# Kernel optimization log

Measured on AMD Instinct MI355X. Metric: run time of the kernel, lower is better.

## Reference

```python
import jax, jax.numpy as jnp
import numpy as np
from jax import lax

DIM = 128
HEADS = 8
B, H, W = 8, 128, 128


def conv1x1(w, x):
    # w: [out_c, in_c], x: [b, in_c, h, w]
    return jnp.einsum('oc,bchw->bohw', w, x)


def setup_inputs() -> dict:
    key = jax.random.key(0)
    ks = jax.random.split(key, 12)
    s = 0.02
    return {
        'x': jax.random.normal(ks[0], (B, DIM, H, W), dtype=jnp.float32),
        'W_qkv': jax.random.normal(ks[1], (3 * DIM, DIM), dtype=jnp.float32) * s,
        'W_dw': jax.random.normal(ks[2], (DIM, 1, 3, 3), dtype=jnp.float32) * s,
        'W_proj_s': jax.random.normal(ks[3], (DIM, DIM), dtype=jnp.float32) * s,
        'scale_s': jnp.ones((HEADS, 1, 1), dtype=jnp.float32),
        'W_ff1': jax.random.normal(ks[4], (DIM, DIM), dtype=jnp.float32) * s,
        'W_ff2': jax.random.normal(ks[5], (DIM, DIM), dtype=jnp.float32) * s,
        'W_proj_f': jax.random.normal(ks[6], (DIM, DIM), dtype=jnp.float32) * s,
        'W_gsf': jax.random.normal(ks[7], (DIM, DIM), dtype=jnp.float32) * s,
        'b_gsf': jnp.zeros((DIM,), dtype=jnp.float32),
        'W_gfs': jax.random.normal(ks[8], (DIM, DIM), dtype=jnp.float32) * s,
        'b_gfs': jnp.zeros((DIM,), dtype=jnp.float32),
    }


def reference(x, W_qkv, W_dw, W_proj_s, scale_s, W_ff1, W_ff2, W_proj_f,
              W_gsf, b_gsf, W_gfs, b_gfs):
    b, c, h, w = x.shape
    head = HEADS
    ch = c // head

    # --- channel self-attention branch ---
    qkv = conv1x1(W_qkv, x)                      # [b, 3c, h, w]
    q_s, k_s, v_s = jnp.split(qkv, 3, axis=1)
    v_s_conv = lax.conv_general_dilated(
        v_s, W_dw, window_strides=(1, 1), padding='SAME',
        feature_group_count=c,
        dimension_numbers=('NCHW', 'OIHW', 'NCHW'))  # depthwise 3x3

    q = q_s.reshape(b, head, ch, h * w)
    k = k_s.reshape(b, head, ch, h * w)
    v = v_s.reshape(b, head, ch, h * w)
    attn = jax.nn.softmax(jnp.einsum('bhcn,bhdn->bhcd', q, k) * scale_s, axis=-1)
    out_s = jnp.einsum('bhcd,bhdn->bhcn', attn, v).reshape(b, c, h, w)
    out_s = conv1x1(W_proj_s, out_s + v_s_conv)

    # --- frequency filter branch ---
    xf = jnp.fft.rfft2(x, norm='ortho')          # complex [b,c,h,w//2+1]
    spatial_weights = conv1x1(W_ff2, jax.nn.gelu(conv1x1(W_ff1, x), approximate=False))
    freq_weights = jnp.fft.rfft2(spatial_weights, norm='ortho')
    out_f = jnp.fft.irfft2(xf * freq_weights, s=(h, w), norm='ortho')
    out_f = conv1x1(W_proj_f, out_f)

    # --- sigmoid-gated fusion ---
    gate_f = jax.nn.sigmoid(conv1x1(W_gsf, out_s) + b_gsf[:, None, None])
    gate_s = jax.nn.sigmoid(conv1x1(W_gfs, out_f) + b_gfs[:, None, None])
    return x + out_s * gate_s + out_f * gate_f
```

## Files before the change

### kernel.cpp

```cpp
#include <hip/hip_runtime.h>
#include <hip/hip_bf16.h>
#include <math.h>

#define HW 16384

typedef __attribute__((ext_vector_type(8))) short bf16x8;
typedef __attribute__((ext_vector_type(4))) float f32x4;

__device__ __forceinline__ unsigned short f2bf(float a)
{
    __hip_bfloat16 h = __float2bfloat16(a);
    return __builtin_bit_cast(unsigned short, h);
}
__device__ __forceinline__ unsigned f2bf_pk(float a, float b)
{
    return (unsigned)f2bf(a) | ((unsigned)f2bf(b) << 16);
}
__device__ __forceinline__ float bf2f(unsigned short u)
{
    return __uint_as_float(((unsigned)u) << 16);
}
__device__ __forceinline__ float sigmoidf_(float v) { return 1.f / (1.f + expf(-v)); }

__device__ __forceinline__ float2 cmul(float2 a, float2 b)
{
    return make_float2(a.x * b.x - a.y * b.y, a.x * b.y + a.y * b.x);
}

__global__ __launch_bounds__(256)
void wprep_k(const float* __restrict__ w0, const float* __restrict__ w1,
             const float* __restrict__ w2, const float* __restrict__ w3,
             const float* __restrict__ w4, const float* __restrict__ w5,
             const float* __restrict__ w6, int4* __restrict__ Wbf4)
{
    int m = blockIdx.x >> 3;
    int slot = (blockIdx.x & 7) * 256 + threadIdx.x;
    const float* src;
    switch (m) {
        case 0: src = w0; break;
        case 1: src = w1; break;
        case 2: src = w2; break;
        case 3: src = w3; break;
        case 4: src = w4; break;
        case 5: src = w5; break;
        default: src = w6; break;
    }
    int o = slot >> 4;
    int c16 = (slot & 15) ^ (o & 7);
    const float* p = src + o * 128 + c16 * 8;
    int4 pk;
    pk.x = f2bf_pk(p[0], p[1]); pk.y = f2bf_pk(p[2], p[3]);
    pk.z = f2bf_pk(p[4], p[5]); pk.w = f2bf_pk(p[6], p[7]);
    Wbf4[m * 2048 + slot] = pk;
}

__global__ __launch_bounds__(256)
void head_k(const float* __restrict__ x, const int4* __restrict__ wv,
            const int4* __restrict__ w1, const int4* __restrict__ w2,
            unsigned short* __restrict__ V, unsigned short* __restrict__ swb)
{
    __shared__ short WL[128 * 128];
    __shared__ short XLx[64 * 128];
    __shared__ short XM[64 * 128];
    int t = threadIdx.x;
    int gb = blockIdx.x;
    int b = gb >> 8;
    int n0 = (gb & 255) << 6;

    #pragma unroll
    for (int it = 0; it < 8; ++it)
        ((int4*)WL)[it * 256 + t] = wv[it * 256 + t];

    const float* inb = x + (size_t)b * 128 * HW + n0;
    int nl = t & 63;
    #pragma unroll
    for (int it = 0; it < 4; ++it) {
        int c8 = (t >> 6) + it * 4;
        float v[8];
        #pragma unroll
        for (int j = 0; j < 8; ++j) v[j] = inb[(size_t)(c8 * 8 + j) * HW + nl];
        int4 p;
        p.x = f2bf_pk(v[0], v[1]); p.y = f2bf_pk(v[2], v[3]);
        p.z = f2bf_pk(v[4], v[5]); p.w = f2bf_pk(v[6], v[7]);
        ((int4*)XLx)[nl * 16 + (c8 ^ (nl & 7))] = p;
    }
    __syncthreads();

    int l = t & 63, w = t >> 6, kg = l >> 4, l15 = l & 15, l7 = l15 & 7;

    f32x4 acc[2][4];
    #pragma unroll
    for (int mf = 0; mf < 2; ++mf)
        #pragma unroll
        for (int nf = 0; nf < 4; ++nf) acc[mf][nf] = (f32x4){0.f, 0.f, 0.f, 0.f};
    #pragma unroll
    for (int ks = 0; ks < 4; ++ks) {
        int ch = ks * 4 + kg;
        bf16x8 A0 = ((const bf16x8*)WL)[(w * 32 + l15) * 16 + (ch ^ l7)];
        bf16x8 A1 = ((const bf16x8*)WL)[(w * 32 + 16 + l15) * 16 + (ch ^ l7)];
        #pragma unroll
        for (int nf = 0; nf < 4; ++nf) {
            bf16x8 Bf = ((const bf16x8*)XLx)[(nf * 16 + l15) * 16 + (ch ^ l7)];
            acc[0][nf] = __builtin_amdgcn_mfma_f32_16x16x32_bf16(A0, Bf, acc[0][nf], 0, 0, 0);
            acc[1][nf] = __builtin_amdgcn_mfma_f32_16x16x32_bf16(A1, Bf, acc[1][nf], 0, 0, 0);
        }
    }
    #pragma unroll
    for (int mf = 0; mf < 2; ++mf)
        #pragma unroll
        for (int nf = 0; nf < 4; ++nf)
            #pragma unroll
            for (int i = 0; i < 4; ++i) {
                int row = w * 32 + mf * 16 + kg * 4 + i;
                int col = n0 + nf * 16 + l15;
                V[((size_t)b * 128 + row) * HW + col] = f2bf(acc[mf][nf][i]);
            }
    __syncthreads();

    #pragma unroll
    for (int it = 0; it < 8; ++it)
        ((int4*)WL)[it * 256 + t] = w1[it * 256 + t];
    __syncthreads();

    #pragma unroll
    for (int mf = 0; mf < 2; ++mf)
        #pragma unroll
        for (int nf = 0; nf < 4; ++nf) acc[mf][nf] = (f32x4){0.f, 0.f, 0.f, 0.f};
    #pragma unroll
    for (int ks = 0; ks < 4; ++ks) {
        int ch = ks * 4 + kg;
        bf16x8 A0 = ((const bf16x8*)WL)[(w * 32 + l15) * 16 + (ch ^ l7)];
        bf16x8 A1 = ((const bf16x8*)WL)[(w * 32 + 16 + l15) * 16 + (ch ^ l7)];
        #pragma unroll
        for (int nf = 0; nf < 4; ++nf) {
            bf16x8 Bf = ((const bf16x8*)XLx)[(nf * 16 + l15) * 16 + (ch ^ l7)];
            acc[0][nf] = __builtin_amdgcn_mfma_f32_16x16x32_bf16(A0, Bf, acc[0][nf], 0, 0, 0);
            acc[1][nf] = __builtin_amdgcn_mfma_f32_16x16x32_bf16(A1, Bf, acc[1][nf], 0, 0, 0);
        }
    }
    __syncthreads();

    #pragma unroll
    for (int it = 0; it < 8; ++it)
        ((int4*)WL)[it * 256 + t] = w2[it * 256 + t];
    #pragma unroll
    for (int mf = 0; mf < 2; ++mf)
        #pragma unroll
        for (int nf = 0; nf < 4; ++nf) {
            float g4[4];
            #pragma unroll
            for (int i = 0; i < 4; ++i) {
                float v = acc[mf][nf][i];
                g4[i] = 0.5f * v * (1.0f + erff(v * 0.70710678118654752f));
            }
            int col = nf * 16 + l15;
            int r0 = w * 32 + mf * 16 + kg * 4;
            int octet = r0 >> 3;
            uint2 pk2;
            pk2.x = f2bf_pk(g4[0], g4[1]);
            pk2.y = f2bf_pk(g4[2], g4[3]);
            ((uint2*)XM)[(col * 16 + (octet ^ (col & 7))) * 2 + (kg & 1)] = pk2;
        }
    __syncthreads();

    f32x4 acc2[2][4];
    #pragma unroll
    for (int mf = 0; mf < 2; ++mf)
        #pragma unroll
        for (int nf = 0; nf < 4; ++nf) acc2[mf][nf] = (f32x4){0.f, 0.f, 0.f, 0.f};
    #pragma unroll
    for (int ks = 0; ks < 4; ++ks) {
        int ch = ks * 4 + kg;
        bf16x8 A0 = ((const bf16x8*)WL)[(w * 32 + l15) * 16 + (ch ^ l7)];
        bf16x8 A1 = ((const bf16x8*)WL)[(w * 32 + 16 + l15) * 16 + (ch ^ l7)];
        #pragma unroll
        for (int nf = 0; nf < 4; ++nf) {
            bf16x8 Bf = ((const bf16x8*)XM)[(nf * 16 + l15) * 16 + (ch ^ l7)];
            acc2[0][nf] = __builtin_amdgcn_mfma_f32_16x16x32_bf16(A0, Bf, acc2[0][nf], 0, 0, 0);
            acc2[1][nf] = __builtin_amdgcn_mfma_f32_16x16x32_bf16(A1, Bf, acc2[1][nf], 0, 0, 0);
        }
    }
    #pragma unroll
    for (int mf = 0; mf < 2; ++mf)
        #pragma unroll
        for (int nf = 0; nf < 4; ++nf)
            #pragma unroll
            for (int i = 0; i < 4; ++i) {
                int row = w * 32 + mf * 16 + kg * 4 + i;
                int col = n0 + nf * 16 + l15;
                swb[((size_t)b * 128 + row) * HW + col] = f2bf(acc2[mf][nf][i]);
            }
}

__global__ __launch_bounds__(256)
void conv_mfma_bf_k(const unsigned short* __restrict__ in,
                    const int4* __restrict__ wbf,
                    unsigned short* __restrict__ out)
{
    __shared__ short WL[128 * 128];
    __shared__ short XL[64 * 128];
    int t = threadIdx.x;
    int gb = blockIdx.x;
    int b = gb >> 8;
    int n0 = (gb & 255) << 6;

    #pragma unroll
    for (int it = 0; it < 8; ++it)
        ((int4*)WL)[it * 256 + t] = wbf[it * 256 + t];

    const unsigned short* inb = in + (size_t)b * 128 * HW + n0;
    int nl = t & 63;
    #pragma unroll
    for (int it = 0; it < 4; ++it) {
        int c8 = (t >> 6) + it * 4;
        unsigned u[8];
        #pragma unroll
        for (int j = 0; j < 8; ++j) u[j] = inb[(size_t)(c8 * 8 + j) * HW + nl];
        int4 p;
        p.x = (int)(u[0] | (u[1] << 16)); p.y = (int)(u[2] | (u[3] << 16));
        p.z = (int)(u[4] | (u[5] << 16)); p.w = (int)(u[6] | (u[7] << 16));
        ((int4*)XL)[nl * 16 + (c8 ^ (nl & 7))] = p;
    }
    __syncthreads();

    int l = t & 63, w = t >> 6, kg = l >> 4, l15 = l & 15, l7 = l15 & 7;
    f32x4 acc[2][4];
    #pragma unroll
    for (int mf = 0; mf < 2; ++mf)
        #pragma unroll
        for (int nf = 0; nf < 4; ++nf) acc[mf][nf] = (f32x4){0.f, 0.f, 0.f, 0.f};
    #pragma unroll
    for (int ks = 0; ks < 4; ++ks) {
        int ch = ks * 4 + kg;
        bf16x8 A0 = ((const bf16x8*)WL)[(w * 32 + l15) * 16 + (ch ^ l7)];
        bf16x8 A1 = ((const bf16x8*)WL)[(w * 32 + 16 + l15) * 16 + (ch ^ l7)];
        #pragma unroll
        for (int nf = 0; nf < 4; ++nf) {
            bf16x8 Bf = ((const bf16x8*)XL)[(nf * 16 + l15) * 16 + (ch ^ l7)];
            acc[0][nf] = __builtin_amdgcn_mfma_f32_16x16x32_bf16(A0, Bf, acc[0][nf], 0, 0, 0);
            acc[1][nf] = __builtin_amdgcn_mfma_f32_16x16x32_bf16(A1, Bf, acc[1][nf], 0, 0, 0);
        }
    }
    #pragma unroll
    for (int mf = 0; mf < 2; ++mf)
        #pragma unroll
        for (int nf = 0; nf < 4; ++nf)
            #pragma unroll
            for (int i = 0; i < 4; ++i) {
                int row = w * 32 + mf * 16 + kg * 4 + i;
                int col = n0 + nf * 16 + l15;
                out[((size_t)b * 128 + row) * HW + col] = f2bf(acc[mf][nf][i]);
            }
}

__global__ __launch_bounds__(256)
void dwconv_k(const unsigned short* __restrict__ V, const float* __restrict__ Wdw,
              unsigned short* __restrict__ vcb)
{
    int tid = blockIdx.x * 256 + threadIdx.x;
    int e4 = tid & 4095;
    int bc = tid >> 12;
    int c = bc & 127;
    int y = e4 >> 5;
    int x0 = (e4 & 31) << 2;
    const unsigned short* vin = V + (size_t)bc * HW;
    float wf[9];
    #pragma unroll
    for (int i = 0; i < 9; ++i) wf[i] = Wdw[c * 9 + i];
    float a0 = 0.f, a1 = 0.f, a2 = 0.f, a3 = 0.f;
    #pragma unroll
    for (int dy = 0; dy < 3; ++dy) {
        int yy = y + dy - 1;
        if (yy < 0 || yy > 127) continue;
        const unsigned short* r = vin + yy * 128;
        uint2 mu = *(const uint2*)(r + x0);
        float m0 = bf2f((unsigned short)(mu.x & 0xFFFF));
        float m1 = bf2f((unsigned short)(mu.x >> 16));
        float m2 = bf2f((unsigned short)(mu.y & 0xFFFF));
        float m3 = bf2f((unsigned short)(mu.y >> 16));
        float left  = (x0 > 0)   ? bf2f(r[x0 - 1]) : 0.f;
        float right = (x0 < 124) ? bf2f(r[x0 + 4]) : 0.f;
        float w0 = wf[dy * 3], w1 = wf[dy * 3 + 1], w2 = wf[dy * 3 + 2];
        a0 += w0 * left + w1 * m0 + w2 * m1;
        a1 += w0 * m0   + w1 * m1 + w2 * m2;
        a2 += w0 * m1   + w1 * m2 + w2 * m3;
        a3 += w0 * m2   + w1 * m3 + w2 * right;
    }
    uint2 r2;
    r2.x = f2bf_pk(a0, a1);
    r2.y = f2bf_pk(a2, a3);
    *(uint2*)(vcb + (size_t)bc * HW + y * 128 + x0) = r2;
}

__global__ __launch_bounds__(256)
void gram_mfma_k(const float* __restrict__ x, float* __restrict__ Gp)
{
    __shared__ short XL[128 * 128];
    int t = threadIdx.x;
    int blk = blockIdx.x;
    int b = blk >> 5, ks = blk & 31;
    const float* xb = x + (size_t)b * 128 * HW + ks * 512;
    int l = t & 63, w = t >> 6, kg = l >> 4, l15 = l & 15, l7 = l15 & 7;

    f32x4 acc[2][8];
    #pragma unroll
    for (int mf = 0; mf < 2; ++mf)
        #pragma unroll
        for (int nf = 0; nf < 8; ++nf) acc[mf][nf] = (f32x4){0.f, 0.f, 0.f, 0.f};

    for (int kc = 0; kc < 4; ++kc) {
        __syncthreads();
        #pragma unroll
        for (int it = 0; it < 8; ++it) {
            int g = it * 256 + t;
            int row = g >> 4, oct = g & 15;
            const float* p = xb + (size_t)row * HW + kc * 128 + oct * 8;
            int4 pk;
            pk.x = f2bf_pk(p[0], p[1]); pk.y = f2bf_pk(p[2], p[3]);
            pk.z = f2bf_pk(p[4], p[5]); pk.w = f2bf_pk(p[6], p[7]);
            ((int4*)XL)[row * 16 + (oct ^ (row & 7))] = pk;
        }
        __syncthreads();
        #pragma unroll
        for (int s = 0; s < 4; ++s) {
            int oct = s * 4 + kg;
            bf16x8 A0 = ((const bf16x8*)XL)[(w * 32 + l15) * 16 + (oct ^ l7)];
            bf16x8 A1 = ((const bf16x8*)XL)[(w * 32 + 16 + l15) * 16 + (oct ^ l7)];
            #pragma unroll
            for (int nf = 0; nf < 8; ++nf) {
                bf16x8 Bf = ((const bf16x8*)XL)[(nf * 16 + l15) * 16 + (oct ^ l7)];
                acc[0][nf] = __builtin_amdgcn_mfma_f32_16x16x32_bf16(A0, Bf, acc[0][nf], 0, 0, 0);
                acc[1][nf] = __builtin_amdgcn_mfma_f32_16x16x32_bf16(A1, Bf, acc[1][nf], 0, 0, 0);
            }
        }
    }
    float* gp = Gp + (size_t)blk * 16384;
    #pragma unroll
    for (int mf = 0; mf < 2; ++mf)
        #pragma unroll
        for (int nf = 0; nf < 8; ++nf)
            #pragma unroll
            for (int i = 0; i < 4; ++i) {
                int row = w * 32 + mf * 16 + kg * 4 + i;
                int col = nf * 16 + l15;
                gp[row * 128 + col] = acc[mf][nf][i];
            }
}

__global__ void gram_reduce_k(const float* __restrict__ Gp, float* __restrict__ G)
{
    int idx = blockIdx.x * 256 + threadIdx.x;
    int b = idx >> 14;
    int ij = idx & 16383;
    const float* gp = Gp + (size_t)(b * 32) * 16384 + ij;
    float s = 0.f;
    #pragma unroll
    for (int ks = 0; ks < 32; ++ks) s += gp[(size_t)ks * 16384];
    G[idx] = s;
}

__global__ __launch_bounds__(256)
void attn_s2_k(const float* __restrict__ G, const float* __restrict__ Wqkv,
               const float* __restrict__ scale, float* __restrict__ S)
{
    __shared__ float Wq[16][129];
    __shared__ float Wk[16][129];
    __shared__ float Ts[16][129];
    int bh = blockIdx.x;
    int b = bh >> 3, h = bh & 7;
    int t = threadIdx.x;
    #pragma unroll
    for (int i = 0; i < 8; ++i) {
        int idx = t + i * 256;
        int r = idx >> 7, ci = idx & 127;
        Wq[r][ci] = Wqkv[(size_t)(h * 16 + r) * 128 + ci];
        Wk[r][ci] = Wqkv[(size_t)(128 + h * 16 + r) * 128 + ci];
    }
    __syncthreads();
    const float* Gb = G + (size_t)b * 16384;
    #pragma unroll
    for (int i = 0; i < 8; ++i) {
        int idx = t + i * 256;
        int c = idx >> 7, col = idx & 127;
        float s = 0.f;
        #pragma unroll 8
        for (int ci = 0; ci < 128; ++ci)
            s += Wq[c][ci] * Gb[ci * 128 + col];
        Ts[c][col] = s;
    }
    __syncthreads();
    int c = t >> 4, d = t & 15;
    float s = 0.f;
    #pragma unroll 8
    for (int col = 0; col < 128; ++col)
        s += Ts[c][col] * Wk[d][col];
    s *= scale[h];
    float m = s;
    #pragma unroll
    for (int w = 1; w < 16; w <<= 1)
        m = fmaxf(m, __shfl_xor(m, w, 64));
    float e = expf(s - m);
    float sum = e;
    #pragma unroll
    for (int w = 1; w < 16; w <<= 1)
        sum += __shfl_xor(sum, w, 64);
    S[(size_t)bh * 256 + t] = e / sum;
}

__global__ __launch_bounds__(256)
void proj_s_pv_k(const unsigned short* __restrict__ V,
                 const unsigned short* __restrict__ vcb,
                 const float* __restrict__ S, const int4* __restrict__ wbf,
                 unsigned short* __restrict__ out_s)
{
    __shared__ short WL[128 * 128];
    __shared__ short XL[64 * 128];
    __shared__ float SL[2048];
    int t = threadIdx.x;
    int gb = blockIdx.x;
    int b = gb >> 8;
    int n0 = (gb & 255) << 6;

    #pragma unroll
    for (int it = 0; it < 8; ++it)
        ((int4*)WL)[it * 256 + t] = wbf[it * 256 + t];
    #pragma unroll
    for (int i = 0; i < 8; ++i)
        SL[i * 256 + t] = S[(size_t)b * 2048 + i * 256 + t];
    __syncthreads();

    int col = t & 63, w = t >> 6;
    #pragma unroll
    for (int hh = 0; hh < 2; ++hh) {
        int h = w * 2 + hh;
        float v[16];
        #pragma unroll
        for (int d = 0; d < 16; ++d)
            v[d] = bf2f(V[((size_t)(b * 128 + h * 16 + d)) * HW + n0 + col]);
        float o[16];
        #pragma unroll
        for (int c = 0; c < 16; ++c) {
            const float* sl = SL + h * 256 + c * 16;
            float s = 0.f;
            #pragma unroll
            for (int d = 0; d < 16; ++d) s += sl[d] * v[d];
            o[c] = s + bf2f(vcb[((size_t)(b * 128 + h * 16 + c)) * HW + n0 + col]);
        }
        #pragma unroll
        for (int oc = 0; oc < 2; ++oc) {
            int octet = h * 2 + oc;
            int4 p;
            p.x = f2bf_pk(o[oc * 8 + 0], o[oc * 8 + 1]);
            p.y = f2bf_pk(o[oc * 8 + 2], o[oc * 8 + 3]);
            p.z = f2bf_pk(o[oc * 8 + 4], o[oc * 8 + 5]);
            p.w = f2bf_pk(o[oc * 8 + 6], o[oc * 8 + 7]);
            ((int4*)XL)[col * 16 + (octet ^ (col & 7))] = p;
        }
    }
    __syncthreads();

    int l = t & 63, kg = l >> 4, l15 = l & 15, l7 = l15 & 7;
    f32x4 acc[2][4];
    #pragma unroll
    for (int mf = 0; mf < 2; ++mf)
        #pragma unroll
        for (int nf = 0; nf < 4; ++nf) acc[mf][nf] = (f32x4){0.f, 0.f, 0.f, 0.f};
    #pragma unroll
    for (int ks = 0; ks < 4; ++ks) {
        int ch = ks * 4 + kg;
        bf16x8 A0 = ((const bf16x8*)WL)[(w * 32 + l15) * 16 + (ch ^ l7)];
        bf16x8 A1 = ((const bf16x8*)WL)[(w * 32 + 16 + l15) * 16 + (ch ^ l7)];
        #pragma unroll
        for (int nf = 0; nf < 4; ++nf) {
            bf16x8 Bf = ((const bf16x8*)XL)[(nf * 16 + l15) * 16 + (ch ^ l7)];
            acc[0][nf] = __builtin_amdgcn_mfma_f32_16x16x32_bf16(A0, Bf, acc[0][nf], 0, 0, 0);
            acc[1][nf] = __builtin_amdgcn_mfma_f32_16x16x32_bf16(A1, Bf, acc[1][nf], 0, 0, 0);
        }
    }
    #pragma unroll
    for (int mf = 0; mf < 2; ++mf)
        #pragma unroll
        for (int nf = 0; nf < 4; ++nf)
            #pragma unroll
            for (int i = 0; i < 4; ++i) {
                int row = w * 32 + mf * 16 + kg * 4 + i;
                int colg = n0 + nf * 16 + l15;
                out_s[((size_t)b * 128 + row) * HW + colg] = f2bf(acc[mf][nf][i]);
            }
}

__global__ __launch_bounds__(256)
void fuse2_k(const float* __restrict__ x, const unsigned short* __restrict__ outs,
             const unsigned short* __restrict__ outf,
             const int4* __restrict__ wgsf_bf, const float* __restrict__ bgsf,
             const int4* __restrict__ wgfs_bf, const float* __restrict__ bgfs,
             float* __restrict__ out)
{
    __shared__ short WS[64 * 128];
    __shared__ short WF[64 * 128];
    __shared__ short XS[64 * 128];
    __shared__ short XF[64 * 128];
    int t = threadIdx.x;
    int gb = blockIdx.x;
    int xcd = gb & 7, ii = gb >> 3;
    int T = xcd * 256 + (ii >> 1);
    int half = ii & 1;
    int b = T >> 8;
    int n0 = (T & 255) << 6;

    #pragma unroll
    for (int it = 0; it < 4; ++it) {
        ((int4*)WS)[it * 256 + t] = wgsf_bf[half * 1024 + it * 256 + t];
        ((int4*)WF)[it * 256 + t] = wgfs_bf[half * 1024 + it * 256 + t];
    }
    const unsigned short* sb = outs + (size_t)b * 128 * HW + n0;
    const unsigned short* fb = outf + (size_t)b * 128 * HW + n0;
    int nl = t & 63;
    #pragma unroll
    for (int it = 0; it < 4; ++it) {
        int c8 = (t >> 6) + it * 4;
        unsigned us[8], uf[8];
        #pragma unroll
        for (int j = 0; j < 8; ++j) {
            size_t a = (size_t)(c8 * 8 + j) * HW + nl;
            us[j] = sb[a];
            uf[j] = fb[a];
        }
        int4 ps, pf;
        ps.x = (int)(us[0] | (us[1] << 16)); ps.y = (int)(us[2] | (us[3] << 16));
        ps.z = (int)(us[4] | (us[5] << 16)); ps.w = (int)(us[6] | (us[7] << 16));
        pf.x = (int)(uf[0] | (uf[1] << 16)); pf.y = (int)(uf[2] | (uf[3] << 16));
        pf.z = (int)(uf[4] | (uf[5] << 16)); pf.w = (int)(uf[6] | (uf[7] << 16));
        ((int4*)XS)[nl * 16 + (c8 ^ (nl & 7))] = ps;
        ((int4*)XF)[nl * 16 + (c8 ^ (nl & 7))] = pf;
    }
    __syncthreads();

    int l = t & 63, w = t >> 6, kg = l >> 4, l15 = l & 15, l7 = l15 & 7;
    f32x4 aS[4], aF[4];
    #pragma unroll
    for (int nf = 0; nf < 4; ++nf) {
        aS[nf] = (f32x4){0.f, 0.f, 0.f, 0.f};
        aF[nf] = (f32x4){0.f, 0.f, 0.f, 0.f};
    }
    #pragma unroll
    for (int ks = 0; ks < 4; ++ks) {
        int ch = ks * 4 + kg;
        bf16x8 As = ((const bf16x8*)WS)[(w * 16 + l15) * 16 + (ch ^ l7)];
        bf16x8 Af = ((const bf16x8*)WF)[(w * 16 + l15) * 16 + (ch ^ l7)];
        #pragma unroll
        for (int nf = 0; nf < 4; ++nf) {
            bf16x8 Bs = ((const bf16x8*)XS)[(nf * 16 + l15) * 16 + (ch ^ l7)];
            bf16x8 Bf = ((const bf16x8*)XF)[(nf * 16 + l15) * 16 + (ch ^ l7)];
            aS[nf] = __builtin_amdgcn_mfma_f32_16x16x32_bf16(As, Bs, aS[nf], 0, 0, 0);
            aF[nf] = __builtin_amdgcn_mfma_f32_16x16x32_bf16(Af, Bf, aF[nf], 0, 0, 0);
        }
    }
    #pragma unroll
    for (int nf = 0; nf < 4; ++nf)
        #pragma unroll
        for (int i = 0; i < 4; ++i) {
            int row = half * 64 + w * 16 + kg * 4 + i;
            int cc = nf * 16 + l15;
            float gf = sigmoidf_(aS[nf][i] + bgsf[row]);
            float gs = sigmoidf_(aF[nf][i] + bgfs[row]);
            size_t gi = ((size_t)(b * 128) + row) * HW + n0 + cc;
            float os = bf2f(outs[gi]);
            float of = bf2f(outf[gi]);
            out[gi] = x[gi] + os * gs + of * gf;
        }
}

__device__ __forceinline__ int ZIX(int r, int j)
{
    return r * 128 + (j ^ ((r & 3) << 3) ^ (((j >> 4) & 3) << 1));
}
__device__ __forceinline__ float2 zld(const unsigned* Z, int r, int j)
{
    unsigned z = Z[ZIX(r, j)];
    return make_float2(bf2f((unsigned short)(z & 0xFFFF)),
                       bf2f((unsigned short)(z >> 16)));
}
__device__ __forceinline__ void zst(unsigned* Z, int r, int j, float2 v)
{
    Z[ZIX(r, j)] = f2bf_pk(v.x, v.y);
}

__device__ __forceinline__ void dft16(float2* v)
{
    const float C1 = 0.92387953251f, S1 = 0.38268343236f, R2 = 0.70710678119f;
    const float2 W16[8] = {
        {1.f, 0.f}, {C1, -S1}, {R2, -R2}, {S1, -C1},
        {0.f, -1.f}, {-S1, -C1}, {-R2, -R2}, {-C1, -S1}};
    #pragma unroll
    for (int i = 0; i < 8; ++i) {
        float2 a = v[i], b = v[i + 8];
        v[i] = make_float2(a.x + b.x, a.y + b.y);
        float2 d = make_float2(a.x - b.x, a.y - b.y);
        v[i + 8] = cmul(d, W16[i]);
    }
    #pragma unroll
    for (int blk = 0; blk < 16; blk += 8)
        #pragma unroll
        for (int i = 0; i < 4; ++i) {
            float2 a = v[blk + i], b = v[blk + i + 4];
            v[blk + i] = make_float2(a.x + b.x, a.y + b.y);
            float2 d = make_float2(a.x - b.x, a.y - b.y);
            v[blk + i + 4] = cmul(d, W16[2 * i]);
        }
    #pragma unroll
    for (int blk = 0; blk < 16; blk += 4) {
        float2 a0 = v[blk], b0 = v[blk + 2];
        v[blk] = make_float2(a0.x + b0.x, a0.y + b0.y);
        v[blk + 2] = make_float2(a0.x - b0.x, a0.y - b0.y);
        float2 a1 = v[blk + 1], b1 = v[blk + 3];
        v[blk + 1] = make_float2(a1.x + b1.x, a1.y + b1.y);
        float2 d = make_float2(a1.x - b1.x, a1.y - b1.y);
        v[blk + 3] = make_float2(d.y, -d.x);
    }
    #pragma unroll
    for (int blk = 0; blk < 16; blk += 2) {
        float2 a = v[blk], b = v[blk + 1];
        v[blk] = make_float2(a.x + b.x, a.y + b.y);
        v[blk + 1] = make_float2(a.x - b.x, a.y - b.y);
    }
}

__device__ __forceinline__ void dft8(float2* v)
{
    const float R2 = 0.70710678119f;
    const float2 W8[4] = {{1.f, 0.f}, {R2, -R2}, {0.f, -1.f}, {-R2, -R2}};
    #pragma unroll
    for (int i = 0; i < 4; ++i) {
        float2 a = v[i], b = v[i + 4];
        v[i] = make_float2(a.x + b.x, a.y + b.y);
        float2 d = make_float2(a.x - b.x, a.y - b.y);
        v[i + 4] = cmul(d, W8[i]);
    }
    #pragma unroll
    for (int blk = 0; blk < 8; blk += 4) {
        float2 a0 = v[blk], b0 = v[blk + 2];
        v[blk] = make_float2(a0.x + b0.x, a0.y + b0.y);
        v[blk + 2] = make_float2(a0.x - b0.x, a0.y - b0.y);
        float2 a1 = v[blk + 1], b1 = v[blk + 3];
        v[blk + 1] = make_float2(a1.x + b1.x, a1.y + b1.y);
        float2 d = make_float2(a1.x - b1.x, a1.y - b1.y);
        v[blk + 3] = make_float2(d.y, -d.x);
    }
    #pragma unroll
    for (int blk = 0; blk < 8; blk += 2) {
        float2 a = v[blk], b = v[blk + 1];
        v[blk] = make_float2(a.x + b.x, a.y + b.y);
        v[blk + 1] = make_float2(a.x - b.x, a.y - b.y);
    }
}

__device__ __forceinline__ void fft_line_row(unsigned* Z, const float2* tw,
                                             int row, int n2)
{
    const int BREV4[16] = {0,8,4,12,2,10,6,14,1,9,5,13,3,11,7,15};
    const int BREV3[8] = {0,4,2,6,1,5,3,7};
    float2 v[16];
    #pragma unroll
    for (int n1 = 0; n1 < 16; ++n1) v[n1] = zld(Z, row, 8 * n1 + n2);
    dft16(v);
    #pragma unroll
    for (int p = 0; p < 16; ++p) {
        int k1 = BREV4[p];
        zst(Z, row, 16 * n2 + k1, cmul(v[p], tw[n2 * k1]));
    }
    float2 wa[8], wb[8];
    #pragma unroll
    for (int m = 0; m < 8; ++m) {
        wa[m] = zld(Z, row, 16 * m + n2);
        wb[m] = zld(Z, row, 16 * m + n2 + 8);
    }
    dft8(wa);
    dft8(wb);
    #pragma unroll
    for (int p = 0; p < 8; ++p) {
        zst(Z, row, n2 + 16 * BREV3[p], wa[p]);
        zst(Z, row, n2 + 8 + 16 * BREV3[p], wb[p]);
    }
}

__device__ __forceinline__ void fft_line_col(unsigned* Z, const float2* tw,
                                             int col, int n2)
{
    const int BREV4[16] = {0,8,4,12,2,10,6,14,1,9,5,13,3,11,7,15};
    const int BREV3[8] = {0,4,2,6,1,5,3,7};
    float2 v[16];
    #pragma unroll
    for (int n1 = 0; n1 < 16; ++n1) v[n1] = zld(Z, 8 * n1 + n2, col);
    dft16(v);
    #pragma unroll
    for (int p = 0; p < 16; ++p) {
        int k1 = BREV4[p];
        zst(Z, 16 * n2 + k1, col, cmul(v[p], tw[n2 * k1]));
    }
    float2 wa[8], wb[8];
    #pragma unroll
    for (int m = 0; m < 8; ++m) {
        wa[m] = zld(Z, 16 * m + n2, col);
        wb[m] = zld(Z, 16 * m + n2 + 8, col);
    }
    dft8(wa);
    dft8(wb);
    #pragma unroll
    for (int p = 0; p < 8; ++p) {
        zst(Z, n2 + 16 * BREV3[p], col, wa[p]);
        zst(Z, n2 + 8 + 16 * BREV3[p], col, wb[p]);
    }
}

__global__ __launch_bounds__(256)
void fft_all_k(const float* __restrict__ x, const unsigned short* __restrict__ sw,
               unsigned short* __restrict__ outp)
{
    __shared__ unsigned Z[128 * 128];
    __shared__ float2 tw[128];
    const int BREV3[8] = {0,4,2,6,1,5,3,7};
    int t = threadIdx.x;
    if (t < 128) {
        float sn, cs;
        sincosf(0.049087385212340519f * (float)t, &sn, &cs);
        tw[t] = make_float2(cs, -sn);
    }
    size_t base = (size_t)blockIdx.x * HW;

    #pragma unroll
    for (int i = 0; i < 64; ++i) {
        int idx = t + i * 256;
        int r = idx >> 7, j = idx & 127;
        Z[ZIX(r, j)] = (unsigned)f2bf(x[base + idx]) |
                       ((unsigned)sw[base + idx] << 16);
    }
    __syncthreads();

    int ln = t >> 3, n2 = t & 7;
    #pragma unroll
    for (int it = 0; it < 4; ++it) fft_line_row(Z, tw, it * 32 + ln, n2);
    __syncthreads();
    #pragma unroll
    for (int it = 0; it < 4; ++it) fft_line_col(Z, tw, it * 32 + ln, n2);
    __syncthreads();

    for (int item = t; item < 8194; item += 256) {
        int rA, kA, rB, kB;
        if (item < 8064) {
            rA = 1 + (item >> 7); kA = item & 127;
            rB = 128 - rA; kB = (128 - kA) & 127;
        } else {
            int it2 = item - 8064;
            rA = rB = (it2 < 65) ? 0 : 64;
            kA = (it2 < 65) ? it2 : (it2 - 65);
            kB = (128 - kA) & 127;
        }
        float2 z1 = zld(Z, rA, kA);
        float2 z2 = zld(Z, rB, kB);
        float2 X = make_float2(0.5f * (z1.x + z2.x), 0.5f * (z1.y - z2.y));
        float Dx = z1.x - z2.x, Dy = z1.y + z2.y;
        float2 Wf = make_float2(0.5f * Dy, -0.5f * Dx);
        float2 Y = cmul(X, Wf);
        zst(Z, rA, kA, make_float2(Y.x, -Y.y));
        zst(Z, rB, kB, Y);
    }
    __syncthreads();

    #pragma unroll
    for (int it = 0; it < 4; ++it) fft_line_col(Z, tw, it * 32 + ln, n2);
    __syncthreads();

    const float scale = 1.f / 2097152.f;
    const int BREV4[16] = {0,8,4,12,2,10,6,14,1,9,5,13,3,11,7,15};
    #pragma unroll
    for (int it = 0; it < 4; ++it) {
        int row = it * 32 + ln;
        float2 v[16];
        #pragma unroll
        for (int n1 = 0; n1 < 16; ++n1) v[n1] = zld(Z, row, 8 * n1 + n2);
        dft16(v);
        #pragma unroll
        for (int p = 0; p < 16; ++p) {
            int k1 = BREV4[p];
            zst(Z, row, 16 * n2 + k1, cmul(v[p], tw[n2 * k1]));
        }
        float2 wa[8], wb[8];
        #pragma unroll
        for (int m = 0; m < 8; ++m) {
            wa[m] = zld(Z, row, 16 * m + n2);
            wb[m] = zld(Z, row, 16 * m + n2 + 8);
        }
        dft8(wa);
        dft8(wb);
        #pragma unroll
        for (int p = 0; p < 8; ++p) {
            outp[base + row * 128 + n2 + 16 * BREV3[p]] = f2bf(wa[p].x * scale);
            outp[base + row * 128 + n2 + 8 + 16 * BREV3[p]] = f2bf(wb[p].x * scale);
        }
    }
}

extern "C" void kernel_launch(void* const* d_in, const int* in_sizes, int n_in,
                              void* d_out, int out_size, void* d_ws, size_t ws_size,
                              hipStream_t stream)
{
    const float* x        = (const float*)d_in[0];
    const float* W_qkv    = (const float*)d_in[1];
    const float* W_dw     = (const float*)d_in[2];
    const float* W_proj_s = (const float*)d_in[3];
    const float* scale_s  = (const float*)d_in[4];
    const float* W_ff1    = (const float*)d_in[5];
    const float* W_ff2    = (const float*)d_in[6];
    const float* W_proj_f = (const float*)d_in[7];
    const float* W_gsf    = (const float*)d_in[8];
    const float* b_gsf    = (const float*)d_in[9];
    const float* W_gfs    = (const float*)d_in[10];
    const float* b_gfs    = (const float*)d_in[11];
    float* out = (float*)d_out;

    char* ws = (char*)d_ws;
    const size_t MB32 = 33554432ull;
    const size_t MB64 = 67108864ull;
    const size_t MB96 = 100663296ull;
    unsigned short* V     = (unsigned short*)(ws);
    unsigned short* out_s = (unsigned short*)(ws + MB32);
    unsigned short* swb   = (unsigned short*)(ws + MB64);
    unsigned short* pre   = (unsigned short*)(ws + MB64);
    unsigned short* out_fp= (unsigned short*)(ws);
    int4* Wbf4            = (int4*)(ws + MB96);
    unsigned short* vcb   = (unsigned short*)out;
    float* Gp  = out + 8388608;
    float* G   = out + 8388608 + 4194304;
    float* S   = G + 131072;

    wprep_k<<<56, 256, 0, stream>>>(W_qkv + 256 * 128, W_proj_s, W_ff1, W_ff2,
                                    W_proj_f, W_gsf, W_gfs, Wbf4);

    head_k<<<2048, 256, 0, stream>>>(x, Wbf4 + 0 * 2048, Wbf4 + 2 * 2048,
                                     Wbf4 + 3 * 2048, V, swb);

    dwconv_k<<<16384, 256, 0, stream>>>(V, W_dw, vcb);
    gram_mfma_k<<<256, 256, 0, stream>>>(x, Gp);
    gram_reduce_k<<<512, 256, 0, stream>>>(Gp, G);
    attn_s2_k<<<64, 256, 0, stream>>>(G, W_qkv, scale_s, S);
    proj_s_pv_k<<<2048, 256, 0, stream>>>(V, vcb, S, Wbf4 + 1 * 2048, out_s);

    fft_all_k<<<1024, 256, 0, stream>>>(x, swb, pre);
    conv_mfma_bf_k<<<2048, 256, 0, stream>>>(pre, Wbf4 + 4 * 2048, out_fp);

    fuse2_k<<<4096, 256, 0, stream>>>(x, out_s, out_fp,
                                      Wbf4 + 5 * 2048, b_gsf,
                                      Wbf4 + 6 * 2048, b_gfs, out);
}
```

Before: 317.4 us.

## Fuse frequency projection conv into gated fusion tail kernel

Merges the W_proj_f 1x1 conv kernel into the final gating kernel. The projected frequency output stays in registers and LDS instead of being written to and reread from global memory as bf16. Each block now runs three 128x128 GEMMs in sequence, reloading the weights into one shared buffer between them. This adds syncs and the full weight reload, and it halves the grid to 2048 blocks. The diff also changes the LDS swizzle in ZIX, apparently to reduce bank conflicts in the FFT kernel.

```diff
diff --git a/kernel.cpp b/kernel.cpp
--- a/kernel.cpp
+++ b/kernel.cpp
@@ -189,67 +189,6 @@
                 int row = w * 32 + mf * 16 + kg * 4 + i;
                 int col = n0 + nf * 16 + l15;
                 swb[((size_t)b * 128 + row) * HW + col] = f2bf(acc2[mf][nf][i]);
-            }
-}
-
-__global__ __launch_bounds__(256)
-void conv_mfma_bf_k(const unsigned short* __restrict__ in,
-                    const int4* __restrict__ wbf,
-                    unsigned short* __restrict__ out)
-{
-    __shared__ short WL[128 * 128];
-    __shared__ short XL[64 * 128];
-    int t = threadIdx.x;
-    int gb = blockIdx.x;
-    int b = gb >> 8;
-    int n0 = (gb & 255) << 6;
-
-    #pragma unroll
-    for (int it = 0; it < 8; ++it)
-        ((int4*)WL)[it * 256 + t] = wbf[it * 256 + t];
-
-    const unsigned short* inb = in + (size_t)b * 128 * HW + n0;
-    int nl = t & 63;
-    #pragma unroll
-    for (int it = 0; it < 4; ++it) {
-        int c8 = (t >> 6) + it * 4;
-        unsigned u[8];
-        #pragma unroll
-        for (int j = 0; j < 8; ++j) u[j] = inb[(size_t)(c8 * 8 + j) * HW + nl];
-        int4 p;
-        p.x = (int)(u[0] | (u[1] << 16)); p.y = (int)(u[2] | (u[3] << 16));
-        p.z = (int)(u[4] | (u[5] << 16)); p.w = (int)(u[6] | (u[7] << 16));
-        ((int4*)XL)[nl * 16 + (c8 ^ (nl & 7))] = p;
-    }
-    __syncthreads();
-
-    int l = t & 63, w = t >> 6, kg = l >> 4, l15 = l & 15, l7 = l15 & 7;
-    f32x4 acc[2][4];
-    #pragma unroll
-    for (int mf = 0; mf < 2; ++mf)
-        #pragma unroll
-        for (int nf = 0; nf < 4; ++nf) acc[mf][nf] = (f32x4){0.f, 0.f, 0.f, 0.f};
-    #pragma unroll
-    for (int ks = 0; ks < 4; ++ks) {
-        int ch = ks * 4 + kg;
-        bf16x8 A0 = ((const bf16x8*)WL)[(w * 32 + l15) * 16 + (ch ^ l7)];
-        bf16x8 A1 = ((const bf16x8*)WL)[(w * 32 + 16 + l15) * 16 + (ch ^ l7)];
-        #pragma unroll
-        for (int nf = 0; nf < 4; ++nf) {
-            bf16x8 Bf = ((const bf16x8*)XL)[(nf * 16 + l15) * 16 + (ch ^ l7)];
-            acc[0][nf] = __builtin_amdgcn_mfma_f32_16x16x32_bf16(A0, Bf, acc[0][nf], 0, 0, 0);
-            acc[1][nf] = __builtin_amdgcn_mfma_f32_16x16x32_bf16(A1, Bf, acc[1][nf], 0, 0, 0);
-        }
-    }
-    #pragma unroll
-    for (int mf = 0; mf < 2; ++mf)
-        #pragma unroll
-        for (int nf = 0; nf < 4; ++nf)
-            #pragma unroll
-            for (int i = 0; i < 4; ++i) {
-                int row = w * 32 + mf * 16 + kg * 4 + i;
-                int col = n0 + nf * 16 + l15;
-                out[((size_t)b * 128 + row) * HW + col] = f2bf(acc[mf][nf][i]);
             }
 }
 
@@ -490,90 +429,149 @@
 }
 
 __global__ __launch_bounds__(256)
-void fuse2_k(const float* __restrict__ x, const unsigned short* __restrict__ outs,
-             const unsigned short* __restrict__ outf,
-             const int4* __restrict__ wgsf_bf, const float* __restrict__ bgsf,
-             const int4* __restrict__ wgfs_bf, const float* __restrict__ bgfs,
-             float* __restrict__ out)
-{
-    __shared__ short WS[64 * 128];
-    __shared__ short WF[64 * 128];
+void tail_k(const float* __restrict__ x, const unsigned short* __restrict__ outs,
+            const unsigned short* __restrict__ pre,
+            const int4* __restrict__ wpf,
+            const int4* __restrict__ wgsf, const float* __restrict__ bgsf,
+            const int4* __restrict__ wgfs, const float* __restrict__ bgfs,
+            float* __restrict__ out)
+{
+    __shared__ short WL[128 * 128];
+    __shared__ short XP[64 * 128];
     __shared__ short XS[64 * 128];
-    __shared__ short XF[64 * 128];
     int t = threadIdx.x;
     int gb = blockIdx.x;
-    int xcd = gb & 7, ii = gb >> 3;
-    int T = xcd * 256 + (ii >> 1);
-    int half = ii & 1;
+    int T = (gb & 7) * 256 + (gb >> 3);
     int b = T >> 8;
     int n0 = (T & 255) << 6;
 
     #pragma unroll
-    for (int it = 0; it < 4; ++it) {
-        ((int4*)WS)[it * 256 + t] = wgsf_bf[half * 1024 + it * 256 + t];
-        ((int4*)WF)[it * 256 + t] = wgfs_bf[half * 1024 + it * 256 + t];
-    }
+    for (int it = 0; it < 8; ++it)
+        ((int4*)WL)[it * 256 + t] = wpf[it * 256 + t];
+
+    const unsigned short* pb = pre + (size_t)b * 128 * HW + n0;
     const unsigned short* sb = outs + (size_t)b * 128 * HW + n0;
-    const unsigned short* fb = outf + (size_t)b * 128 * HW + n0;
     int nl = t & 63;
     #pragma unroll
     for (int it = 0; it < 4; ++it) {
         int c8 = (t >> 6) + it * 4;
-        unsigned us[8], uf[8];
+        unsigned up[8], us[8];
         #pragma unroll
         for (int j = 0; j < 8; ++j) {
             size_t a = (size_t)(c8 * 8 + j) * HW + nl;
+            up[j] = pb[a];
             us[j] = sb[a];
-            uf[j] = fb[a];
-        }
-        int4 ps, pf;
+        }
+        int4 pp, ps;
+        pp.x = (int)(up[0] | (up[1] << 16)); pp.y = (int)(up[2] | (up[3] << 16));
+        pp.z = (int)(up[4] | (up[5] << 16)); pp.w = (int)(up[6] | (up[7] << 16));
         ps.x = (int)(us[0] | (us[1] << 16)); ps.y = (int)(us[2] | (us[3] << 16));
         ps.z = (int)(us[4] | (us[5] << 16)); ps.w = (int)(us[6] | (us[7] << 16));
-        pf.x = (int)(uf[0] | (uf[1] << 16)); pf.y = (int)(uf[2] | (uf[3] << 16));
-        pf.z = (int)(uf[4] | (uf[5] << 16)); pf.w = (int)(uf[6] | (uf[7] << 16));
+        ((int4*)XP)[nl * 16 + (c8 ^ (nl & 7))] = pp;
         ((int4*)XS)[nl * 16 + (c8 ^ (nl & 7))] = ps;
-        ((int4*)XF)[nl * 16 + (c8 ^ (nl & 7))] = pf;
     }
     __syncthreads();
 
     int l = t & 63, w = t >> 6, kg = l >> 4, l15 = l & 15, l7 = l15 & 7;
-    f32x4 aS[4], aF[4];
-    #pragma unroll
-    for (int nf = 0; nf < 4; ++nf) {
-        aS[nf] = (f32x4){0.f, 0.f, 0.f, 0.f};
-        aF[nf] = (f32x4){0.f, 0.f, 0.f, 0.f};
-    }
+
+    f32x4 accF[2][4];
+    #pragma unroll
+    for (int mf = 0; mf < 2; ++mf)
+        #pragma unroll
+        for (int nf = 0; nf < 4; ++nf) accF[mf][nf] = (f32x4){0.f, 0.f, 0.f, 0.f};
     #pragma unroll
     for (int ks = 0; ks < 4; ++ks) {
         int ch = ks * 4 + kg;
-        bf16x8 As = ((const bf16x8*)WS)[(w * 16 + l15) * 16 + (ch ^ l7)];
-        bf16x8 Af = ((const bf16x8*)WF)[(w * 16 + l15) * 16 + (ch ^ l7)];
+        bf16x8 A0 = ((const bf16x8*)WL)[(w * 32 + l15) * 16 + (ch ^ l7)];
+        bf16x8 A1 = ((const bf16x8*)WL)[(w * 32 + 16 + l15) * 16 + (ch ^ l7)];
         #pragma unroll
         for (int nf = 0; nf < 4; ++nf) {
-            bf16x8 Bs = ((const bf16x8*)XS)[(nf * 16 + l15) * 16 + (ch ^ l7)];
-            bf16x8 Bf = ((const bf16x8*)XF)[(nf * 16 + l15) * 16 + (ch ^ l7)];
-            aS[nf] = __builtin_amdgcn_mfma_f32_16x16x32_bf16(As, Bs, aS[nf], 0, 0, 0);
-            aF[nf] = __builtin_amdgcn_mfma_f32_16x16x32_bf16(Af, Bf, aF[nf], 0, 0, 0);
-        }
-    }
-    #pragma unroll
-    for (int nf = 0; nf < 4; ++nf)
-        #pragma unroll
-        for (int i = 0; i < 4; ++i) {
-            int row = half * 64 + w * 16 + kg * 4 + i;
-            int cc = nf * 16 + l15;
-            float gf = sigmoidf_(aS[nf][i] + bgsf[row]);
-            float gs = sigmoidf_(aF[nf][i] + bgfs[row]);
-            size_t gi = ((size_t)(b * 128) + row) * HW + n0 + cc;
-            float os = bf2f(outs[gi]);
-            float of = bf2f(outf[gi]);
-            out[gi] = x[gi] + os * gs + of * gf;
-        }
+            bf16x8 Bf = ((const bf16x8*)XP)[(nf * 16 + l15) * 16 + (ch ^ l7)];
+            accF[0][nf] = __builtin_amdgcn_mfma_f32_16x16x32_bf16(A0, Bf, accF[0][nf], 0, 0, 0);
+            accF[1][nf] = __builtin_amdgcn_mfma_f32_16x16x32_bf16(A1, Bf, accF[1][nf], 0, 0, 0);
+        }
+    }
+    __syncthreads();
+
+    #pragma unroll
+    for (int it = 0; it < 8; ++it)
+        ((int4*)WL)[it * 256 + t] = wgsf[it * 256 + t];
+    #pragma unroll
+    for (int mf = 0; mf < 2; ++mf)
+        #pragma unroll
+        for (int nf = 0; nf < 4; ++nf) {
+            int col = nf * 16 + l15;
+            int r0 = w * 32 + mf * 16 + kg * 4;
+            int octet = r0 >> 3;
+            uint2 pk2;
+            pk2.x = f2bf_pk(accF[mf][nf][0], accF[mf][nf][1]);
+            pk2.y = f2bf_pk(accF[mf][nf][2], accF[mf][nf][3]);
+            ((uint2*)XP)[(col * 16 + (octet ^ (col & 7))) * 2 + (kg & 1)] = pk2;
+        }
+    __syncthreads();
+
+    f32x4 aS[2][4];
+    #pragma unroll
+    for (int mf = 0; mf < 2; ++mf)
+        #pragma unroll
+        for (int nf = 0; nf < 4; ++nf) aS[mf][nf] = (f32x4){0.f, 0.f, 0.f, 0.f};
+    #pragma unroll
+    for (int ks = 0; ks < 4; ++ks) {
+        int ch = ks * 4 + kg;
+        bf16x8 A0 = ((const bf16x8*)WL)[(w * 32 + l15) * 16 + (ch ^ l7)];
+        bf16x8 A1 = ((const bf16x8*)WL)[(w * 32 + 16 + l15) * 16 + (ch ^ l7)];
+        #pragma unroll
+        for (int nf = 0; nf < 4; ++nf) {
+            bf16x8 Bf = ((const bf16x8*)XS)[(nf * 16 + l15) * 16 + (ch ^ l7)];
+            aS[0][nf] = __builtin_amdgcn_mfma_f32_16x16x32_bf16(A0, Bf, aS[0][nf], 0, 0, 0);
+            aS[1][nf] = __builtin_amdgcn_mfma_f32_16x16x32_bf16(A1, Bf, aS[1][nf], 0, 0, 0);
+        }
+    }
+    __syncthreads();
+
+    #pragma unroll
+    for (int it = 0; it < 8; ++it)
+        ((int4*)WL)[it * 256 + t] = wgfs[it * 256 + t];
+    __syncthreads();
+
+    f32x4 aF[2][4];
+    #pragma unroll
+    for (int mf = 0; mf < 2; ++mf)
+        #pragma unroll
+        for (int nf = 0; nf < 4; ++nf) aF[mf][nf] = (f32x4){0.f, 0.f, 0.f, 0.f};
+    #pragma unroll
+    for (int ks = 0; ks < 4; ++ks) {
+        int ch = ks * 4 + kg;
+        bf16x8 A0 = ((const bf16x8*)WL)[(w * 32 + l15) * 16 + (ch ^ l7)];
+        bf16x8 A1 = ((const bf16x8*)WL)[(w * 32 + 16 + l15) * 16 + (ch ^ l7)];
+        #pragma unroll
+        for (int nf = 0; nf < 4; ++nf) {
+            bf16x8 Bf = ((const bf16x8*)XP)[(nf * 16 + l15) * 16 + (ch ^ l7)];
+            aF[0][nf] = __builtin_amdgcn_mfma_f32_16x16x32_bf16(A0, Bf, aF[0][nf], 0, 0, 0);
+            aF[1][nf] = __builtin_amdgcn_mfma_f32_16x16x32_bf16(A1, Bf, aF[1][nf], 0, 0, 0);
+        }
+    }
+
+    #pragma unroll
+    for (int mf = 0; mf < 2; ++mf)
+        #pragma unroll
+        for (int nf = 0; nf < 4; ++nf)
+            #pragma unroll
+            for (int i = 0; i < 4; ++i) {
+                int row = w * 32 + mf * 16 + kg * 4 + i;
+                int cc = n0 + nf * 16 + l15;
+                float gf = sigmoidf_(aS[mf][nf][i] + bgsf[row]);
+                float gs = sigmoidf_(aF[mf][nf][i] + bgfs[row]);
+                size_t gi = ((size_t)(b * 128) + row) * HW + cc;
+                float os = bf2f(outs[gi]);
+                float of = accF[mf][nf][i];
+                out[gi] = x[gi] + os * gs + of * gf;
+            }
 }
 
 __device__ __forceinline__ int ZIX(int r, int j)
 {
-    return r * 128 + (j ^ ((r & 3) << 3) ^ (((j >> 4) & 3) << 1));
+    return r * 128 + (j ^ (((r ^ (r >> 4)) & 3) << 3) ^ (((j >> 4) & 3) << 1));
 }
 __device__ __forceinline__ float2 zld(const unsigned* Z, int r, int j)
 {
@@ -827,7 +825,6 @@
     unsigned short* out_s = (unsigned short*)(ws + MB32);
     unsigned short* swb   = (unsigned short*)(ws + MB64);
     unsigned short* pre   = (unsigned short*)(ws + MB64);
-    unsigned short* out_fp= (unsigned short*)(ws);
     int4* Wbf4            = (int4*)(ws + MB96);
     unsigned short* vcb   = (unsigned short*)out;
     float* Gp  = out + 8388608;
@@ -847,9 +844,8 @@
     proj_s_pv_k<<<2048, 256, 0, stream>>>(V, vcb, S, Wbf4 + 1 * 2048, out_s);
 
     fft_all_k<<<1024, 256, 0, stream>>>(x, swb, pre);
-    conv_mfma_bf_k<<<2048, 256, 0, stream>>>(pre, Wbf4 + 4 * 2048, out_fp);
-
-    fuse2_k<<<4096, 256, 0, stream>>>(x, out_s, out_fp,
-                                      Wbf4 + 5 * 2048, b_gsf,
-                                      Wbf4 + 6 * 2048, b_gfs, out);
-}
+
+    tail_k<<<2048, 256, 0, stream>>>(x, out_s, pre, Wbf4 + 4 * 2048,
+                                     Wbf4 + 5 * 2048, b_gsf,
+                                     Wbf4 + 6 * 2048, b_gfs, out);
+}
```

Result: faster. 300.4 us (-5.4%).
